# Kernel tuning notes

Hardware: AMD Instinct MI355X
Metric: run time of the kernel (lower is better)

The kernel has to match this reference:

```python
import jax, jax.numpy as jnp
import numpy as np

B, S, H, NH = 2, 2048, 1024, 16
HD = H // NH  # head_dim = 64
ROPE_BASE = 10000.0


def _rope(x):
    # x: [B, NH, S, HD]; LLaMA-style half-split rotary embedding
    s, d = x.shape[2], x.shape[3]
    inv_freq = 1.0 / (ROPE_BASE ** (jnp.arange(0, d, 2, dtype=jnp.float32) / d))  # [d/2]
    ang = jnp.arange(s, dtype=jnp.float32)[:, None] * inv_freq[None, :]            # [S, d/2]
    cos, sin = jnp.cos(ang), jnp.sin(ang)
    x1, x2 = x[..., : d // 2], x[..., d // 2:]
    return jnp.concatenate([x1 * cos - x2 * sin, x1 * sin + x2 * cos], axis=-1)


def setup_inputs() -> dict:
    key = jax.random.key(0)
    ks = jax.random.split(key, 9)
    hidden_states = jax.random.normal(ks[0], (B, S, H), dtype=jnp.float32)
    # causal mask: True = attend
    causal = jnp.tril(jnp.ones((S, S), dtype=bool))
    attention_mask = jnp.broadcast_to(causal[None, None, :, :], (B, 1, S, S))
    std = 0.02
    wq = jax.random.normal(ks[1], (H, NH * HD), dtype=jnp.float32) * std
    wk = jax.random.normal(ks[2], (H, NH * HD), dtype=jnp.float32) * std
    wv = jax.random.normal(ks[3], (H, NH * HD), dtype=jnp.float32) * std
    wo = jax.random.normal(ks[4], (NH * HD, H), dtype=jnp.float32) * std
    bq = jnp.zeros((NH * HD,), dtype=jnp.float32)
    bk = jnp.zeros((NH * HD,), dtype=jnp.float32)
    bv = jnp.zeros((NH * HD,), dtype=jnp.float32)
    bo = jnp.zeros((H,), dtype=jnp.float32)
    return {"hidden_states": hidden_states, "attention_mask": attention_mask,
            "wq": wq, "bq": bq, "wk": wk, "bk": bk, "wv": wv, "bv": bv,
            "wo": wo, "bo": bo}


def _split_heads(x):
    b, s, _ = x.shape
    return jnp.transpose(x.reshape(b, s, NH, HD), (0, 2, 1, 3))


def reference(hidden_states, attention_mask, wq, bq, wk, bk, wv, bv, wo, bo):
    q = _split_heads(hidden_states @ wq + bq)  # [B,NH,S,HD]
    k = _split_heads(hidden_states @ wk + bk)
    v = _split_heads(hidden_states @ wv + bv)
    q = _rope(q)
    k = _rope(k)
    scores = jnp.einsum('bhqd,bhkd->bhqk', q, k) / jnp.sqrt(jnp.float32(HD))
    scores = jnp.where(attention_mask, scores, jnp.float32(-1e9))
    weights = jax.nn.softmax(scores, axis=-1)
    attn = jnp.einsum('bhqk,bhkv->bhqv', weights, v)  # [B,NH,S,HD]
    attn = jnp.transpose(attn, (0, 2, 1, 3)).reshape(hidden_states.shape[0], attn.shape[2], H)
    return attn @ wo + bo
```

## Files before the change

kernel.cpp:

```cpp
#include <hip/hip_runtime.h>
#include <math.h>

typedef short bf16x8 __attribute__((ext_vector_type(8)));
typedef short bf16x4 __attribute__((ext_vector_type(4)));
typedef float f32x4  __attribute__((ext_vector_type(4)));

__device__ __forceinline__ unsigned short f2bf(float f) {
    union { float f; unsigned u; } v; v.f = f;
    unsigned r = v.u + 0x7FFFu + ((v.u >> 16) & 1u);
    return (unsigned short)(r >> 16);
}

__device__ __forceinline__ unsigned cvt_pk_bf16(float a, float b) {
    unsigned r;
    asm("v_cvt_pk_bf16_f32 %0, %1, %2" : "=v"(r) : "v"(a), "v"(b));
    return r;
}

#define GLDS16(gp, lp) __builtin_amdgcn_global_load_lds( \
    (const __attribute__((address_space(1))) void*)(gp), \
    (__attribute__((address_space(3))) void*)(lp), 16, 0, 0)


__global__ __launch_bounds__(256)
void prep(const float* __restrict__ X, unsigned short* __restrict__ Xb,
          const float* __restrict__ w0, const float* __restrict__ w1,
          const float* __restrict__ w2, const float* __restrict__ w3,
          unsigned short* o0, unsigned short* o1,
          unsigned short* o2, unsigned short* o3)
{
    const int z = blockIdx.z;
    if (z >= 4) {
        const int lb = (z - 4) * 256 + blockIdx.y * 16 + blockIdx.x;
        const size_t t = (size_t)lb * 256 + threadIdx.x;
        const float4 a = *(const float4*)(X + t * 8);
        const float4 b = *(const float4*)(X + t * 8 + 4);
        unsigned short u[8] = { f2bf(a.x), f2bf(a.y), f2bf(a.z), f2bf(a.w),
                                f2bf(b.x), f2bf(b.y), f2bf(b.z), f2bf(b.w) };
        *(int4*)(Xb + t * 8) = *(int4*)u;
        return;
    }
    const float* W; unsigned short* O;
    switch (z) {
        case 0: W = w0; O = o0; break;
        case 1: W = w1; O = o1; break;
        case 2: W = w2; O = o2; break;
        default: W = w3; O = o3; break;
    }
    __shared__ float T[64][65];
    const int tid = threadIdx.x;
    const int n0 = blockIdx.x * 64, k0 = blockIdx.y * 64;
    #pragma unroll
    for (int i = 0; i < 4; i++) {
        const int k = (tid >> 4) + i * 16, n4 = (tid & 15) * 4;
        const float4 v = *(const float4*)(W + (size_t)(k0 + k) * 1024 + n0 + n4);
        T[k][n4] = v.x; T[k][n4+1] = v.y; T[k][n4+2] = v.z; T[k][n4+3] = v.w;
    }
    __syncthreads();
    if (z == 3) {
        #pragma unroll
        for (int i = 0; i < 4; i++) {
            const int n = (tid >> 4) + i * 16, k4 = (tid & 15) * 4;
            unsigned short u[4];
            #pragma unroll
            for (int j = 0; j < 4; j++) {
                const int q = k4 + j;
                const int p = (q & 3) * 16 + (q >> 2);
                const int d = (p & 3) * 16 + (p >> 2);
                u[j] = f2bf(T[d][n]);
            }
            *(int2*)(O + (size_t)(n0 + n) * 1024 + k0 + k4) = *(int2*)u;
        }
    } else {
        #pragma unroll
        for (int i = 0; i < 4; i++) {
            const int n = (tid >> 4) + i * 16, k4 = (tid & 15) * 4;
            unsigned short u[4] = { f2bf(T[k4][n]), f2bf(T[k4+1][n]),
                                    f2bf(T[k4+2][n]), f2bf(T[k4+3][n]) };
            *(int2*)(O + (size_t)(n0 + n) * 1024 + k0 + k4) = *(int2*)u;
        }
    }
}

__global__ __launch_bounds__(256)
void qkv_gemm(const unsigned short* __restrict__ Xb,
              const unsigned short* __restrict__ Wtq, const unsigned short* __restrict__ Wtk,
              const unsigned short* __restrict__ Wtv,
              const float* __restrict__ bq, const float* __restrict__ bk,
              const float* __restrict__ bv,
              unsigned short* __restrict__ Qb, unsigned short* __restrict__ Kb,
              unsigned short* __restrict__ Vtb)
{
    const unsigned short* Wt; const float* bias; unsigned short* Out;
    const int z = blockIdx.z;
    if (z == 0)      { Wt = Wtq; bias = bq; Out = Qb; }
    else if (z == 1) { Wt = Wtk; bias = bk; Out = Kb; }
    else             { Wt = Wtv; bias = bv; Out = Vtb; }

    __shared__ unsigned short Sh[128 * 72];
    unsigned short* As = Sh;
    unsigned short* Bs = Sh + 128 * 32;
    unsigned short* T  = Sh;

    const int tid = threadIdx.x, lane = tid & 63, w = tid >> 6;
    const int quad = lane >> 4, c = lane & 15;
    const int wr = w >> 1, wc = w & 1;
    const int m0 = blockIdx.x * 128, n0 = blockIdx.y * 128;
    const int srow = lane >> 2, scol = (lane & 3) * 8;

    f32x4 acc[4][4];
    #pragma unroll
    for (int i = 0; i < 4; i++)
        #pragma unroll
        for (int j = 0; j < 4; j++) acc[i][j] = (f32x4){0.f, 0.f, 0.f, 0.f};

    for (int k0 = 0; k0 < 1024; k0 += 32) {
        #pragma unroll
        for (int j = 0; j < 2; j++) {
            const int r = w * 32 + j * 16;
            GLDS16(Xb + (size_t)(m0 + r + srow) * 1024 + k0 + scol, &As[r * 32]);
            GLDS16(Wt + (size_t)(n0 + r + srow) * 1024 + k0 + scol, &Bs[r * 32]);
        }
        __syncthreads();
        bf16x8 af[4], bf[4];
        #pragma unroll
        for (int rt = 0; rt < 4; rt++)
            af[rt] = *(const bf16x8*)&As[(wr * 64 + rt * 16 + c) * 32 + quad * 8];
        #pragma unroll
        for (int nt = 0; nt < 4; nt++)
            bf[nt] = *(const bf16x8*)&Bs[(wc * 64 + nt * 16 + c) * 32 + quad * 8];
        #pragma unroll
        for (int rt = 0; rt < 4; rt++)
            #pragma unroll
            for (int nt = 0; nt < 4; nt++)
                acc[rt][nt] = __builtin_amdgcn_mfma_f32_16x16x32_bf16(af[rt], bf[nt], acc[rt][nt], 0, 0, 0);
        __syncthreads();
    }

    float bv4[4];
    #pragma unroll
    for (int nt = 0; nt < 4; nt++) bv4[nt] = bias[n0 + wc * 64 + nt * 16 + c];

    if (z == 2) {
        const int b = m0 >> 11, sb = m0 & 2047;
        const int hgbase = n0 >> 6;
        #pragma unroll
        for (int h = 0; h < 2; h++) {
            if (wc == h) {
                #pragma unroll
                for (int rt = 0; rt < 4; rt++)
                    #pragma unroll
                    for (int reg = 0; reg < 4; reg++) {
                        const int s = wr * 64 + rt * 16 + quad * 4 + reg;
                        unsigned short u[4];
                        #pragma unroll
                        for (int nt = 0; nt < 4; nt++)
                            u[nt] = f2bf(acc[rt][nt][reg] + bv4[nt]);
                        *(int2*)&T[s * 72 + c * 4] = *(int2*)u;
                    }
            }
            __syncthreads();
            const int p = tid >> 2, s8 = (tid & 3) * 32;
            unsigned short* dstb = Vtb + ((size_t)(b * 16 + hgbase + h) * 64 + p) * 2048 + sb;
            #pragma unroll
            for (int jj = 0; jj < 32; jj += 8) {
                unsigned short u[8];
                #pragma unroll
                for (int j = 0; j < 8; j++) u[j] = T[(s8 + jj + j) * 72 + p];
                *(int4*)(dstb + s8 + jj) = *(int4*)u;
            }
            __syncthreads();
        }
        return;
    }

    const float kLn = 9.210340371976184f / 32.0f;
    const float TWO_PI_INV = 0.15915494309189535f;
    const float rv0 = expf(-(float)c * kLn) * TWO_PI_INV;
    const float rv1 = expf(-(float)(c + 16) * kLn) * TWO_PI_INV;
    const float qscale = (z == 0) ? 0.125f : 1.0f;

    #pragma unroll
    for (int rt = 0; rt < 4; rt++) {
        #pragma unroll
        for (int reg = 0; reg < 4; reg++) {
            const int m = m0 + wr * 64 + rt * 16 + quad * 4 + reg;
            const int b = m >> 11, s = m & 2047;
            float x0 = acc[rt][0][reg] + bv4[0];
            float x1 = acc[rt][1][reg] + bv4[1];
            float x2 = acc[rt][2][reg] + bv4[2];
            float x3 = acc[rt][3][reg] + bv4[3];
            float r0 = (float)s * rv0;  r0 -= floorf(r0);
            float r1 = (float)s * rv1;  r1 -= floorf(r1);
            const float sn0 = __builtin_amdgcn_sinf(r0);
            const float cs0 = __builtin_amdgcn_cosf(r0);
            const float sn1 = __builtin_amdgcn_sinf(r1);
            const float cs1 = __builtin_amdgcn_cosf(r1);
            const float y0 = (x0 * cs0 - x2 * sn0) * qscale;
            const float y2 = (x0 * sn0 + x2 * cs0) * qscale;
            const float y1 = (x1 * cs1 - x3 * sn1) * qscale;
            const float y3 = (x1 * sn1 + x3 * cs1) * qscale;
            const int h = (n0 + wc * 64) >> 6;
            unsigned short u[4] = { f2bf(y0), f2bf(y1), f2bf(y2), f2bf(y3) };
            unsigned short* dst = Out + ((size_t)(b * 16 + h) * 2048 + s) * 64;
            *(int2*)(dst + c * 4) = *(int2*)u;
        }
    }
}

__global__ __launch_bounds__(256)
void out_gemm(const unsigned short* __restrict__ Ab, const unsigned short* __restrict__ Wto,
              const float* __restrict__ bo, float* __restrict__ Out)
{
    __shared__ unsigned short As[64 * 32];
    __shared__ unsigned short Bs[128 * 32];
    const int tid = threadIdx.x, lane = tid & 63, w = tid >> 6;
    const int quad = lane >> 4, c = lane & 15;
    const int wr = w >> 1, wc = w & 1;
    const int m0 = blockIdx.x * 64, n0 = blockIdx.y * 128;
    const int srow = lane >> 2, scol = (lane & 3) * 8;

    f32x4 acc[2][4];
    #pragma unroll
    for (int i = 0; i < 2; i++)
        #pragma unroll
        for (int j = 0; j < 4; j++) acc[i][j] = (f32x4){0.f, 0.f, 0.f, 0.f};

    for (int k0 = 0; k0 < 1024; k0 += 32) {
        {
            const int r = w * 16;
            GLDS16(Ab + (size_t)(m0 + r + srow) * 1024 + k0 + scol, &As[r * 32]);
        }
        #pragma unroll
        for (int j = 0; j < 2; j++) {
            const int r = w * 32 + j * 16;
            GLDS16(Wto + (size_t)(n0 + r + srow) * 1024 + k0 + scol, &Bs[r * 32]);
        }
        __syncthreads();
        bf16x8 af[2], bf[4];
        #pragma unroll
        for (int rt = 0; rt < 2; rt++)
            af[rt] = *(const bf16x8*)&As[(wr * 32 + rt * 16 + c) * 32 + quad * 8];
        #pragma unroll
        for (int nt = 0; nt < 4; nt++)
            bf[nt] = *(const bf16x8*)&Bs[(wc * 64 + nt * 16 + c) * 32 + quad * 8];
        #pragma unroll
        for (int rt = 0; rt < 2; rt++)
            #pragma unroll
            for (int nt = 0; nt < 4; nt++)
                acc[rt][nt] = __builtin_amdgcn_mfma_f32_16x16x32_bf16(af[rt], bf[nt], acc[rt][nt], 0, 0, 0);
        __syncthreads();
    }
    #pragma unroll
    for (int rt = 0; rt < 2; rt++) {
        #pragma unroll
        for (int reg = 0; reg < 4; reg++) {
            const int m = m0 + wr * 32 + rt * 16 + quad * 4 + reg;
            #pragma unroll
            for (int nt = 0; nt < 4; nt++) {
                const int n = n0 + wc * 64 + nt * 16 + c;
                Out[(size_t)m * 1024 + n] = acc[rt][nt][reg] + bo[n];
            }
        }
    }
}

__global__ __launch_bounds__(512)
void attn_part(const unsigned short* __restrict__ Qb, const unsigned short* __restrict__ Kb,
               const unsigned short* __restrict__ Vtb, unsigned short* __restrict__ Ab,
               float* __restrict__ Opart, float* __restrict__ Lpart)
{
    __shared__ unsigned short Ks[64 * 72];
    __shared__ unsigned short Vs[64 * 72];

    const int tid = threadIdx.x, w = tid >> 6, lane = tid & 63;
    const int quad = lane >> 4, c = lane & 15;
    const int bh = blockIdx.y;
    const int x = blockIdx.x;
    const int i = (int)((0x014425566377ULL >> (4 * x)) & 15);
    const int chunk = (594 >> x) & 1;
    const int len = ((i >= 4) ? 2 : 4) * (i + 1);
    const int start = chunk ? len : 0;
    const int q0 = i * 256;
    const bool complete = (i <= 3);
    const size_t base = (size_t)bh * 2048 * 64;

    bf16x8 on;
    #pragma unroll
    for (int ii = 0; ii < 8; ii++) on[ii] = (short)0x3F80;

    const int qbase = q0 + w * 32;
    const size_t qoffA = base + (size_t)(qbase + c) * 64;
    const size_t qoffB = base + (size_t)(qbase + 16 + c) * 64;
    const bf16x8 qfA0 = *(const bf16x8*)(Qb + qoffA + quad * 8);
    const bf16x8 qfA1 = *(const bf16x8*)(Qb + qoffA + 32 + quad * 8);
    const bf16x8 qfB0 = *(const bf16x8*)(Qb + qoffB + quad * 8);
    const bf16x8 qfB1 = *(const bf16x8*)(Qb + qoffB + 32 + quad * 8);

    f32x4 OA[4], OB[4], OsA, OsB;
    OsA = (f32x4){0.f, 0.f, 0.f, 0.f};
    OsB = (f32x4){0.f, 0.f, 0.f, 0.f};
    #pragma unroll
    for (int nt = 0; nt < 4; nt++) { OA[nt] = OsA; OB[nt] = OsA; }

    const int rs = tid >> 3, c8 = (tid & 7) * 8;

    int k0 = start * 64;
    int4 kreg = *(const int4*)(Kb  + base + (size_t)(k0 + rs) * 64 + c8);
    int4 vreg = *(const int4*)(Vtb + base + (size_t)rs * 2048 + k0 + c8);

    union P8 { bf16x8 v8; unsigned wd[4]; };
    union V8 { bf16x8 v8; bf16x4 v4[2]; };

    for (int t = 0; t < len; t++, k0 += 64) {
        *(int4*)&Ks[(size_t)rs * 72 + c8] = kreg;
        *(int4*)&Vs[(size_t)rs * 72 + c8] = vreg;
        __syncthreads();

        if (t + 1 < len) {
            const int kn = k0 + 64;
            kreg = *(const int4*)(Kb  + base + (size_t)(kn + rs) * 64 + c8);
            vreg = *(const int4*)(Vtb + base + (size_t)rs * 2048 + kn + c8);
        }

        if (k0 <= qbase + 31) {
            const int qrowA = qbase + c;
            const int qrowB = qbase + 16 + c;
            const bool nmA = (k0 + 63) > qbase;
            const bool nmB = (k0 + 63) > (qbase + 16);
            P8 paA0, paA1, paB0, paB1;
            __builtin_amdgcn_s_setprio(1);
            #pragma unroll
            for (int nt = 0; nt < 4; nt++) {
                const bf16x8 kf0 = *(const bf16x8*)&Ks[(nt * 16 + c) * 72 + quad * 8];
                const bf16x8 kf1 = *(const bf16x8*)&Ks[(nt * 16 + c) * 72 + 32 + quad * 8];
                f32x4 sA = (f32x4){0.f, 0.f, 0.f, 0.f};
                f32x4 sB = sA;
                sA = __builtin_amdgcn_mfma_f32_16x16x32_bf16(kf0, qfA0, sA, 0, 0, 0);
                sA = __builtin_amdgcn_mfma_f32_16x16x32_bf16(kf1, qfA1, sA, 0, 0, 0);
                sB = __builtin_amdgcn_mfma_f32_16x16x32_bf16(kf0, qfB0, sB, 0, 0, 0);
                sB = __builtin_amdgcn_mfma_f32_16x16x32_bf16(kf1, qfB1, sB, 0, 0, 0);
                const int keyb = k0 + nt * 16 + quad * 4;
                float pA[4], pB[4];
                #pragma unroll
                for (int reg = 0; reg < 4; reg++) {
                    float va = __expf(sA[reg]);
                    if (nmA && (keyb + reg > qrowA)) va = 0.f;
                    pA[reg] = va;
                    float vb = __expf(sB[reg]);
                    if (nmB && (keyb + reg > qrowB)) vb = 0.f;
                    pB[reg] = vb;
                }
                const unsigned waA = cvt_pk_bf16(pA[0], pA[1]);
                const unsigned wbA = cvt_pk_bf16(pA[2], pA[3]);
                const unsigned waB = cvt_pk_bf16(pB[0], pB[1]);
                const unsigned wbB = cvt_pk_bf16(pB[2], pB[3]);
                if (nt < 2) {
                    paA0.wd[2 * nt] = waA;     paA0.wd[2 * nt + 1] = wbA;
                    paB0.wd[2 * nt] = waB;     paB0.wd[2 * nt + 1] = wbB;
                } else {
                    paA1.wd[2 * (nt-2)] = waA; paA1.wd[2 * (nt-2) + 1] = wbA;
                    paB1.wd[2 * (nt-2)] = waB; paB1.wd[2 * (nt-2) + 1] = wbB;
                }
            }

            #pragma unroll
            for (int nt = 0; nt < 4; nt++) {
                const int pr = (nt * 16 + c) * 72 + 4 * quad;
                V8 vb0, vb1;
                vb0.v4[0] = *(const bf16x4*)&Vs[pr];
                vb0.v4[1] = *(const bf16x4*)&Vs[pr + 16];
                vb1.v4[0] = *(const bf16x4*)&Vs[pr + 32];
                vb1.v4[1] = *(const bf16x4*)&Vs[pr + 48];
                OA[nt] = __builtin_amdgcn_mfma_f32_16x16x32_bf16(paA0.v8, vb0.v8, OA[nt], 0, 0, 0);
                OA[nt] = __builtin_amdgcn_mfma_f32_16x16x32_bf16(paA1.v8, vb1.v8, OA[nt], 0, 0, 0);
                OB[nt] = __builtin_amdgcn_mfma_f32_16x16x32_bf16(paB0.v8, vb0.v8, OB[nt], 0, 0, 0);
                OB[nt] = __builtin_amdgcn_mfma_f32_16x16x32_bf16(paB1.v8, vb1.v8, OB[nt], 0, 0, 0);
            }
            OsA = __builtin_amdgcn_mfma_f32_16x16x32_bf16(paA0.v8, on, OsA, 0, 0, 0);
            OsA = __builtin_amdgcn_mfma_f32_16x16x32_bf16(paA1.v8, on, OsA, 0, 0, 0);
            OsB = __builtin_amdgcn_mfma_f32_16x16x32_bf16(paB0.v8, on, OsB, 0, 0, 0);
            OsB = __builtin_amdgcn_mfma_f32_16x16x32_bf16(paB1.v8, on, OsB, 0, 0, 0);
            __builtin_amdgcn_s_setprio(0);
        }
        __syncthreads();
    }

    if (complete) {
        const int b = bh >> 4, h = bh & 15;
        #pragma unroll
        for (int reg = 0; reg < 4; reg++) {
            const float invA = 1.0f / OsA[reg];
            const int qA = qbase + quad * 4 + reg;
            unsigned short uA[4];
            #pragma unroll
            for (int nt = 0; nt < 4; nt++) uA[nt] = f2bf(OA[nt][reg] * invA);
            unsigned short* dA = Ab + ((size_t)(b * 2048 + qA)) * 1024 + h * 64;
            *(int2*)(dA + c * 4) = *(int2*)uA;

            const float invB = 1.0f / OsB[reg];
            const int qB = qbase + 16 + quad * 4 + reg;
            unsigned short uB[4];
            #pragma unroll
            for (int nt = 0; nt < 4; nt++) uB[nt] = f2bf(OB[nt][reg] * invB);
            unsigned short* dB = Ab + ((size_t)(b * 2048 + qB)) * 1024 + h * 64;
            *(int2*)(dB + c * 4) = *(int2*)uB;
        }
    } else {
        const int slot = (i - 4) * 2 + chunk;
        float* Op = Opart + ((size_t)bh * 8 + slot) * 16384;
        float* Lp = Lpart + (size_t)bh * 2048 + (size_t)slot * 256;
        #pragma unroll
        for (int reg = 0; reg < 4; reg++) {
            const int rowA = w * 32 + quad * 4 + reg;
            float4 oA = make_float4(OA[0][reg], OA[1][reg], OA[2][reg], OA[3][reg]);
            *(float4*)(Op + (size_t)rowA * 64 + c * 4) = oA;
            if (c == 0) Lp[rowA] = OsA[reg];

            const int rowB = rowA + 16;
            float4 oB = make_float4(OB[0][reg], OB[1][reg], OB[2][reg], OB[3][reg]);
            *(float4*)(Op + (size_t)rowB * 64 + c * 4) = oB;
            if (c == 0) Lp[rowB] = OsB[reg];
        }
    }
}

__global__ __launch_bounds__(256)
void attn_combine(const float* __restrict__ Opart, const float* __restrict__ Lpart,
                  unsigned short* __restrict__ Ab)
{
    const int tid = threadIdx.x;
    const int j = blockIdx.x, bh = blockIdx.y;
    const int i = 4 + (j >> 1), half = j & 1;
    const int slot0 = (i - 4) * 2;
    const int q0 = i * 256 + half * 128;
    const size_t s0 = ((size_t)bh * 8 + slot0) * 16384 + (size_t)half * 128 * 64;
    const size_t l0 = (size_t)bh * 2048 + (size_t)slot0 * 256 + half * 128;

    __shared__ float linv[128];
    if (tid < 128) linv[tid] = 1.0f / (Lpart[l0 + tid] + Lpart[l0 + 256 + tid]);
    __syncthreads();

    const int row = tid >> 1, col0 = (tid & 1) * 32;
    const float inv = linv[row];
    const int b = bh >> 4, h = bh & 15;
    const int q = q0 + row;
    unsigned short* dst = Ab + ((size_t)(b * 2048 + q)) * 1024 + h * 64 + col0;
    #pragma unroll
    for (int c4 = 0; c4 < 32; c4 += 4) {
        const float4 a  = *(const float4*)(Opart + s0 + (size_t)row * 64 + col0 + c4);
        const float4 bb = *(const float4*)(Opart + s0 + 16384 + (size_t)row * 64 + col0 + c4);
        dst[c4 + 0] = f2bf((a.x + bb.x) * inv);
        dst[c4 + 1] = f2bf((a.y + bb.y) * inv);
        dst[c4 + 2] = f2bf((a.z + bb.z) * inv);
        dst[c4 + 3] = f2bf((a.w + bb.w) * inv);
    }
}

extern "C" void kernel_launch(void* const* d_in, const int* in_sizes, int n_in,
                              void* d_out, int out_size, void* d_ws, size_t ws_size,
                              hipStream_t stream)
{
    const float* X  = (const float*)d_in[0];
    const float* wq = (const float*)d_in[2];
    const float* bq = (const float*)d_in[3];
    const float* wk = (const float*)d_in[4];
    const float* bk = (const float*)d_in[5];
    const float* wv = (const float*)d_in[6];
    const float* bv = (const float*)d_in[7];
    const float* wo = (const float*)d_in[8];
    const float* bo = (const float*)d_in[9];

    unsigned short* ws = (unsigned short*)d_ws;
    const size_t M1 = 1024 * 1024;
    unsigned short* Xb  = ws;
    unsigned short* Wtq = Xb  + 4 * M1;
    unsigned short* Wtk = Wtq + M1;
    unsigned short* Wtv = Wtk + M1;
    unsigned short* Wto = Wtv + M1;
    unsigned short* Qb  = Wto + M1;
    unsigned short* Kb  = Qb  + 4 * M1;
    unsigned short* Vtb = Kb  + 4 * M1;
    unsigned short* Ab  = Vtb + 4 * M1;
    float* Opart = (float*)(Ab + 4 * M1);
    float* Lpart = Opart + (size_t)32 * 8 * 16384;

    prep        <<<dim3(16, 16, 12), 256, 0, stream>>>(X, Xb, wq, wk, wv, wo,
                                                       Wtq, Wtk, Wtv, Wto);
    qkv_gemm    <<<dim3(32, 8, 3), 256, 0, stream>>>(Xb, Wtq, Wtk, Wtv, bq, bk, bv,
                                                     Qb, Kb, Vtb);
    attn_part   <<<dim3(12, 32), 512, 0, stream>>>(Qb, Kb, Vtb, Ab, Opart, Lpart);
    attn_combine<<<dim3(8, 32), 256, 0, stream>>>(Opart, Lpart, Ab);
    out_gemm    <<<dim3(64, 8), 256, 0, stream>>>(Ab, Wto, bo, (float*)d_out);
}
```

Measured before the change: 208.3 us.

## Double-buffer QKV GEMM LDS tiles and XOR-swizzle LDS reads

The QKV projection GEMM now keeps two LDS buffers and issues the global-to-LDS loads for the next K tile before running the MFMAs on the current one, so load latency overlaps with compute. It also XOR-swizzles the 16-byte chunk column on both the store and read side to reduce LDS bank conflicts on fragment loads. LDS use grows to 32 KB per block, which may lower occupancy. Correctness depends on the loads into the other buffer completing before the next iteration's barrier.

```diff
diff --git a/kernel.cpp b/kernel.cpp
--- a/kernel.cpp
+++ b/kernel.cpp
@@ -97,16 +97,16 @@
     else if (z == 1) { Wt = Wtk; bias = bk; Out = Kb; }
     else             { Wt = Wtv; bias = bv; Out = Vtb; }
 
-    __shared__ unsigned short Sh[128 * 72];
-    unsigned short* As = Sh;
-    unsigned short* Bs = Sh + 128 * 32;
-    unsigned short* T  = Sh;
+    __shared__ unsigned short Sh[16384];
+    unsigned short* T = Sh;
 
     const int tid = threadIdx.x, lane = tid & 63, w = tid >> 6;
     const int quad = lane >> 4, c = lane & 15;
     const int wr = w >> 1, wc = w & 1;
     const int m0 = blockIdx.x * 128, n0 = blockIdx.y * 128;
-    const int srow = lane >> 2, scol = (lane & 3) * 8;
+    const int srow = lane >> 2;
+    const int scol = ((lane & 3) ^ ((lane >> 3) & 3)) * 8;
+    const int sA = (quad ^ ((c >> 1) & 3)) * 8;
 
     f32x4 acc[4][4];
     #pragma unroll
@@ -114,27 +114,43 @@
         #pragma unroll
         for (int j = 0; j < 4; j++) acc[i][j] = (f32x4){0.f, 0.f, 0.f, 0.f};
 
-    for (int k0 = 0; k0 < 1024; k0 += 32) {
-        #pragma unroll
-        for (int j = 0; j < 2; j++) {
-            const int r = w * 32 + j * 16;
-            GLDS16(Xb + (size_t)(m0 + r + srow) * 1024 + k0 + scol, &As[r * 32]);
-            GLDS16(Wt + (size_t)(n0 + r + srow) * 1024 + k0 + scol, &Bs[r * 32]);
-        }
-        __syncthreads();
+    #pragma unroll
+    for (int j = 0; j < 2; j++) {
+        const int r = w * 32 + j * 16;
+        GLDS16(Xb + (size_t)(m0 + r + srow) * 1024 + 0 + scol, &Sh[r * 32]);
+        GLDS16(Wt + (size_t)(n0 + r + srow) * 1024 + 0 + scol, &Sh[4096 + r * 32]);
+    }
+    __syncthreads();
+
+    int cur = 0;
+    for (int t = 0; t < 32; ++t) {
+        if (t + 1 < 32) {
+            const int kn = (t + 1) * 32;
+            unsigned short* An = Sh + (cur ^ 1) * 8192;
+            unsigned short* Bn = An + 4096;
+            #pragma unroll
+            for (int j = 0; j < 2; j++) {
+                const int r = w * 32 + j * 16;
+                GLDS16(Xb + (size_t)(m0 + r + srow) * 1024 + kn + scol, &An[r * 32]);
+                GLDS16(Wt + (size_t)(n0 + r + srow) * 1024 + kn + scol, &Bn[r * 32]);
+            }
+        }
+        const unsigned short* As = Sh + cur * 8192;
+        const unsigned short* Bs = As + 4096;
         bf16x8 af[4], bf[4];
         #pragma unroll
         for (int rt = 0; rt < 4; rt++)
-            af[rt] = *(const bf16x8*)&As[(wr * 64 + rt * 16 + c) * 32 + quad * 8];
+            af[rt] = *(const bf16x8*)&As[(wr * 64 + rt * 16 + c) * 32 + sA];
         #pragma unroll
         for (int nt = 0; nt < 4; nt++)
-            bf[nt] = *(const bf16x8*)&Bs[(wc * 64 + nt * 16 + c) * 32 + quad * 8];
+            bf[nt] = *(const bf16x8*)&Bs[(wc * 64 + nt * 16 + c) * 32 + sA];
         #pragma unroll
         for (int rt = 0; rt < 4; rt++)
             #pragma unroll
             for (int nt = 0; nt < 4; nt++)
                 acc[rt][nt] = __builtin_amdgcn_mfma_f32_16x16x32_bf16(af[rt], bf[nt], acc[rt][nt], 0, 0, 0);
         __syncthreads();
+        cur ^= 1;
     }
 
     float bv4[4];
```

Result: slower. 212.7 us (+2.1%).
